# Optimization experiments

Measured on AMD Instinct MI355X. Metric: run time of the kernel, lower is better.

The kernel has to match this reference:

```python
import jax, jax.numpy as jnp
import numpy as np

N, E, IN, HID, H, G = 50000, 400000, 128, 16, 11, 64
HC = HID * H  # 176
OUT, NC = 32, 10
EPS = 1e-5


def setup_inputs() -> dict:
    key = jax.random.key(0)
    ks = jax.random.split(key, 20)
    def n(i, shape, s=0.05):
        return jax.random.normal(ks[i], shape, jnp.float32) * s
    inp = {}
    inp["x"] = jax.random.normal(ks[0], (N, IN), jnp.float32)
    inp["edge_index"] = jax.random.randint(ks[1], (2, E), 0, N, dtype=jnp.int32)
    inp["batch"] = jnp.sort(jax.random.randint(ks[2], (N,), 0, G, dtype=jnp.int32))
    inp["W_pre"] = n(3, (IN, HC)); inp["b_pre"] = jnp.zeros((HC,), jnp.float32)
    # GraphNorm params for gn_pre, gn1..gn4 stacked: [5, HC]
    inp["gn_w"] = jnp.ones((5, HC), jnp.float32)
    inp["gn_b"] = jnp.zeros((5, HC), jnp.float32)
    inp["gn_ms"] = jnp.ones((5, HC), jnp.float32)  # mean_scale
    # conv1..conv4 (concat=True) stacked params
    inp["conv_Wl"] = n(4, (4, HC, HC)); inp["conv_Wr"] = n(5, (4, HC, HC))
    inp["conv_att"] = n(6, (4, H, HID))
    inp["conv_b"] = jnp.zeros((4, HC), jnp.float32)
    inp["conv_Wres"] = n(7, (4, HC, HC))
    # conv5 (concat=False -> out dim HID)
    inp["c5_Wl"] = n(8, (HC, HC)); inp["c5_Wr"] = n(9, (HC, HC))
    inp["c5_att"] = n(10, (H, HID))
    inp["c5_b"] = jnp.zeros((HID,), jnp.float32)
    inp["c5_Wres"] = n(11, (HC, HID))
    inp["W_o1"] = n(12, (HID, HID)); inp["b_o1"] = jnp.zeros((HID,), jnp.float32)
    inp["W_o2"] = n(13, (HID, OUT)); inp["b_o2"] = jnp.zeros((OUT,), jnp.float32)
    inp["W_cls"] = n(14, (OUT, NC)); inp["b_cls"] = jnp.zeros((NC,), jnp.float32)
    return inp


def graph_norm(x, w, b, ms, batch, cnt):
    # PyG GraphNorm: out = w * (x - ms*mean) / sqrt(var + eps) + b, stats per graph
    mean = jax.ops.segment_sum(x, batch, G) / cnt  # [G, F]
    xc = x - mean[batch] * ms
    var = jax.ops.segment_sum(xc * xc, batch, G) / cnt
    std = jnp.sqrt(var + EPS)
    return w * xc / std[batch] + b


def gatv2_conv(x, Wl, Wr, att, bias, Wres, src, dst, concat):
    # src/dst already include self-loops (PyG add_self_loops=True)
    xl = (x @ Wl).reshape(N, H, -1)  # source transform [N,H,C]
    xr = (x @ Wr).reshape(N, H, -1)  # target transform [N,H,C]
    e = jax.nn.leaky_relu(xl[src] + xr[dst], 0.2)          # [E',H,C]
    alpha = jnp.einsum('ehc,hc->eh', e, att)               # [E',H]
    amax = jax.ops.segment_max(alpha, dst, N)
    amax = jnp.where(jnp.isfinite(amax), amax, 0.0)
    ex = jnp.exp(alpha - amax[dst])
    den = jax.ops.segment_sum(ex, dst, N)
    a = ex / (den[dst] + 1e-16)
    out = jax.ops.segment_sum(xl[src] * a[..., None], dst, N)  # [N,H,C]
    out = out.reshape(N, -1) if concat else out.mean(axis=1)
    return out + x @ Wres + bias


def reference(x, edge_index, batch, W_pre, b_pre, gn_w, gn_b, gn_ms,
              conv_Wl, conv_Wr, conv_att, conv_b, conv_Wres,
              c5_Wl, c5_Wr, c5_att, c5_b, c5_Wres,
              W_o1, b_o1, W_o2, b_o2, W_cls, b_cls):
    loops = jnp.arange(N, dtype=edge_index.dtype)
    src = jnp.concatenate([edge_index[0], loops])
    dst = jnp.concatenate([edge_index[1], loops])
    cnt = jax.ops.segment_sum(jnp.ones((N, 1), jnp.float32), batch, G)
    cnt = jnp.maximum(cnt, 1.0)  # guard empty graphs

    h = x @ W_pre + b_pre
    h = graph_norm(h, gn_w[0], gn_b[0], gn_ms[0], batch, cnt)
    h = jax.nn.relu(h)
    for i in range(4):
        h = gatv2_conv(h, conv_Wl[i], conv_Wr[i], conv_att[i], conv_b[i],
                       conv_Wres[i], src, dst, concat=True)
        h = graph_norm(h, gn_w[i + 1], gn_b[i + 1], gn_ms[i + 1], batch, cnt)
        h = jax.nn.relu(h)
    h = gatv2_conv(h, c5_Wl, c5_Wr, c5_att, c5_b, c5_Wres, src, dst, concat=False)
    h = jax.nn.relu(h)
    h = jax.nn.relu(h @ W_o1 + b_o1)
    h = jax.nn.relu(h @ W_o2 + b_o2)
    return h @ W_cls + b_cls
```

## Files before the change

kernel.cpp:

```cpp
#include <hip/hip_runtime.h>
#include <math.h>

#define N_NODES 50000
#define N_EDGES 400000
#define IN_F 128
#define HC 176
#define NGRAPH 64
#define NBLK_ATTN 12500
#define NCHUNK 16
#define SQOFF (NGRAPH * NCHUNK * HC)

typedef _Float16 half8 __attribute__((ext_vector_type(8)));
typedef _Float16 half4 __attribute__((ext_vector_type(4)));
typedef _Float16 half2v __attribute__((ext_vector_type(2)));
typedef float floatx4 __attribute__((ext_vector_type(4)));

__device__ inline const _Float16* urow(const _Float16* p, int c) {
  return p + (size_t)(unsigned)__builtin_amdgcn_readfirstlane(c) * HC;
}

#define PREH 45056
#define MATH 67584
#define TOT_PAIRS 495616
#define KCBYTES 22528
#define GX8 49

__global__ void prep_kernel(const float* __restrict__ Wpre,
                            const float* __restrict__ cWl, const float* __restrict__ cWr,
                            const float* __restrict__ cWres,
                            const float* __restrict__ c5Wl, const float* __restrict__ c5Wr,
                            _Float16* __restrict__ wp) {
  int gid = blockIdx.x * 256 + threadIdx.x;
  if (gid >= TOT_PAIRS) return;
  int mat, idx;
  if (gid < 22528) { mat = 0; idx = gid; }
  else { int g = gid - 22528; mat = 1 + g / 33792; idx = g % 33792; }
  int kc = idx / 5632;
  int rem = idx - kc * 5632;
  int ct = rem / 512;
  int li = rem - ct * 512;
  int lane = li >> 3, j = li & 7;
  int k = kc * 32 + ((lane >> 4) << 3) + j;
  int col = ct * 16 + (lane & 15);
  const float* src; int Ksrc; size_t base;
  if (mat == 0) { src = Wpre; Ksrc = 128; base = 0; }
  else if (mat <= 12) {
    int lm = mat - 1; int layer = lm / 3; int sub = lm - layer * 3;
    const float* s = (sub == 0) ? cWl : (sub == 1) ? cWr : cWres;
    src = s + (size_t)layer * HC * HC; Ksrc = HC;
    base = PREH + (size_t)lm * MATH;
  } else {
    src = (mat == 13) ? c5Wl : c5Wr; Ksrc = HC;
    base = PREH + (size_t)12 * MATH + (size_t)(mat - 13) * MATH;
  }
  float v = (k < Ksrc) ? src[(size_t)k * HC + col] : 0.0f;
  _Float16 h = (_Float16)v;
  _Float16 l = (_Float16)(v - (float)h);
  size_t o = base + (size_t)(kc * 11 + ct) * 1024 + li;
  wp[o] = h;
  wp[o + 512] = l;
}

template <int MINW, bool DOSTATS, bool AHALF>
__global__ __launch_bounds__(256, MINW) void gemm_mfma_t(
    const float* __restrict__ A, int M, int K, int nkc, int nmat,
    const _Float16* __restrict__ Wp, int matStride,
    const float* __restrict__ scsh, const int* __restrict__ batch,
    const float* __restrict__ bias0, const float* __restrict__ bias1,
    const float* __restrict__ bias2,
    float* __restrict__ out0, float* __restrict__ out1, float* __restrict__ out2,
    float* __restrict__ stats, int halfMask) {
  __shared__ __align__(16) char smem[2 * KCBYTES];
  const int b = blockIdx.x;
  const int grp = b >> 3, sub = b & 7;
  const int mat = grp % nmat;
  const int tile = ((grp / nmat) << 3) | sub;
  if (tile * 128 >= M) return;
  const _Float16* W = Wp + (size_t)mat * matStride;
  float* outp = (mat == 0) ? out0 : (mat == 1) ? out1 : out2;
  const float* bias = (mat == 0) ? bias0 : (mat == 1) ? bias1 : bias2;
  const bool hOut = (halfMask >> mat) & 1;
  const int tid = threadIdx.x;
  const int lane = tid & 63;
  const int wv = tid >> 6;
  const int m16 = lane & 15, quad = lane >> 4;
  const int kb = quad << 3;
  const int rowBase = tile * 128 + wv * 32;
  const int rA0 = min(rowBase + m16, M - 1);
  const int rA1 = min(rowBase + 16 + m16, M - 1);
  const float* ap0 = A + (size_t)rA0 * K + kb;
  const float* ap1 = A + (size_t)rA1 * K + kb;
  const _Float16* hp0 = (const _Float16*)A + (size_t)rA0 * K + kb;
  const _Float16* hp1 = (const _Float16*)A + (size_t)rA1 * K + kb;
  const float* sc0 = nullptr; const float* sh0 = nullptr;
  const float* sc1 = nullptr; const float* sh1 = nullptr;
  if (scsh) {
    int g0 = batch[rA0], g1 = batch[rA1];
    sc0 = scsh + (size_t)g0 * HC + kb;
    sh0 = scsh + (size_t)(NGRAPH + g0) * HC + kb;
    sc1 = scsh + (size_t)g1 * HC + kb;
    sh1 = scsh + (size_t)(NGRAPH + g1) * HC + kb;
  }

  auto stage = [&](int kc, int buf) {
    const char* src = (const char*)W + (size_t)kc * KCBYTES;
    char* dst = smem + buf * KCBYTES;
#pragma unroll
    for (int i = 0; i < 6; i++) {
      int idx = wv * 6 + i;
      if (idx < 22) {
        __builtin_amdgcn_global_load_lds(
            (const __attribute__((address_space(1))) unsigned int*)(src + idx * 1024 + lane * 16),
            (__attribute__((address_space(3))) unsigned int*)(dst + idx * 1024),
            16, 0, 0);
      }
    }
  };

  floatx4 acc0[11], acc1[11];
#pragma unroll
  for (int ct = 0; ct < 11; ct++)
#pragma unroll
    for (int r = 0; r < 4; r++) { acc0[ct][r] = 0.0f; acc1[ct][r] = 0.0f; }

  stage(0, 0);

  for (int kc = 0; kc < nkc; kc++) {
    const int buf = kc & 1;
    __syncthreads();
    if (kc + 1 < nkc) stage(kc + 1, 1 - buf);

    const int koff = kc << 5;
    float va0[8], va1[8];
    if (koff + kb + 8 <= K) {
      if (AHALF) {
        half8 u = *(const half8*)(hp0 + koff);
        half8 w = *(const half8*)(hp1 + koff);
#pragma unroll
        for (int j = 0; j < 8; j++) { va0[j] = (float)u[j]; va1[j] = (float)w[j]; }
      } else {
        float4 u0 = *(const float4*)(ap0 + koff);
        float4 u1 = *(const float4*)(ap0 + koff + 4);
        float4 w0 = *(const float4*)(ap1 + koff);
        float4 w1 = *(const float4*)(ap1 + koff + 4);
        va0[0] = u0.x; va0[1] = u0.y; va0[2] = u0.z; va0[3] = u0.w;
        va0[4] = u1.x; va0[5] = u1.y; va0[6] = u1.z; va0[7] = u1.w;
        va1[0] = w0.x; va1[1] = w0.y; va1[2] = w0.z; va1[3] = w0.w;
        va1[4] = w1.x; va1[5] = w1.y; va1[6] = w1.z; va1[7] = w1.w;
      }
      if (scsh) {
        float s0[8], h0[8], s1[8], h1[8];
        float4 t;
        t = *(const float4*)(sc0 + koff);     s0[0]=t.x; s0[1]=t.y; s0[2]=t.z; s0[3]=t.w;
        t = *(const float4*)(sc0 + koff + 4); s0[4]=t.x; s0[5]=t.y; s0[6]=t.z; s0[7]=t.w;
        t = *(const float4*)(sh0 + koff);     h0[0]=t.x; h0[1]=t.y; h0[2]=t.z; h0[3]=t.w;
        t = *(const float4*)(sh0 + koff + 4); h0[4]=t.x; h0[5]=t.y; h0[6]=t.z; h0[7]=t.w;
        t = *(const float4*)(sc1 + koff);     s1[0]=t.x; s1[1]=t.y; s1[2]=t.z; s1[3]=t.w;
        t = *(const float4*)(sc1 + koff + 4); s1[4]=t.x; s1[5]=t.y; s1[6]=t.z; s1[7]=t.w;
        t = *(const float4*)(sh1 + koff);     h1[0]=t.x; h1[1]=t.y; h1[2]=t.z; h1[3]=t.w;
        t = *(const float4*)(sh1 + koff + 4); h1[4]=t.x; h1[5]=t.y; h1[6]=t.z; h1[7]=t.w;
#pragma unroll
        for (int j = 0; j < 8; j++) {
          va0[j] = fmaxf(fmaf(va0[j], s0[j], h0[j]), 0.0f);
          va1[j] = fmaxf(fmaf(va1[j], s1[j], h1[j]), 0.0f);
        }
      }
    } else {
#pragma unroll
      for (int j = 0; j < 8; j++) { va0[j] = 0.0f; va1[j] = 0.0f; }
    }
    half8 ah0, al0, ah1, al1;
#pragma unroll
    for (int j = 0; j < 8; j++) {
      _Float16 h = (_Float16)va0[j];
      ah0[j] = h; al0[j] = (_Float16)(va0[j] - (float)h);
      _Float16 g = (_Float16)va1[j];
      ah1[j] = g; al1[j] = (_Float16)(va1[j] - (float)g);
    }
    const char* bbase = smem + buf * KCBYTES + lane * 16;
#pragma unroll
    for (int ct = 0; ct < 11; ct++) {
      half8 bh = *(const half8*)(bbase + ct * 2048);
      half8 bl = *(const half8*)(bbase + ct * 2048 + 1024);
      acc0[ct] = __builtin_amdgcn_mfma_f32_16x16x32_f16(ah0, bh, acc0[ct], 0, 0, 0);
      acc1[ct] = __builtin_amdgcn_mfma_f32_16x16x32_f16(ah1, bh, acc1[ct], 0, 0, 0);
      acc0[ct] = __builtin_amdgcn_mfma_f32_16x16x32_f16(al0, bh, acc0[ct], 0, 0, 0);
      acc1[ct] = __builtin_amdgcn_mfma_f32_16x16x32_f16(al1, bh, acc1[ct], 0, 0, 0);
      acc0[ct] = __builtin_amdgcn_mfma_f32_16x16x32_f16(ah0, bl, acc0[ct], 0, 0, 0);
      acc1[ct] = __builtin_amdgcn_mfma_f32_16x16x32_f16(ah1, bl, acc1[ct], 0, 0, 0);
    }
  }

  float bv[11];
#pragma unroll
  for (int ct = 0; ct < 11; ct++) bv[ct] = bias ? bias[ct * 16 + m16] : 0.0f;
#pragma unroll
  for (int r = 0; r < 4; r++) {
    int row0 = rowBase + (quad << 2) + r;
    if (row0 < M) {
      if (hOut) {
        _Float16* op = (_Float16*)outp + (size_t)row0 * HC + m16;
#pragma unroll
        for (int ct = 0; ct < 11; ct++) op[ct * 16] = (_Float16)(acc0[ct][r] + bv[ct]);
      } else {
        float* op = outp + (size_t)row0 * HC + m16;
#pragma unroll
        for (int ct = 0; ct < 11; ct++) op[ct * 16] = acc0[ct][r] + bv[ct];
      }
    }
    int row1 = row0 + 16;
    if (row1 < M) {
      if (hOut) {
        _Float16* op = (_Float16*)outp + (size_t)row1 * HC + m16;
#pragma unroll
        for (int ct = 0; ct < 11; ct++) op[ct * 16] = (_Float16)(acc1[ct][r] + bv[ct]);
      } else {
        float* op = outp + (size_t)row1 * HC + m16;
#pragma unroll
        for (int ct = 0; ct < 11; ct++) op[ct * 16] = acc1[ct][r] + bv[ct];
      }
    }
  }

  if (DOSTATS) {
    int gTile = batch[tile * 128];
    int lastRow = min(tile * 128 + 127, M - 1);
    bool straddle = (batch[lastRow] != gTile);
    bool validR[8]; bool otherR[8];
#pragma unroll
    for (int r = 0; r < 4; r++) {
      int row0 = rowBase + (quad << 2) + r;
      validR[r] = (row0 < M);
      otherR[r] = validR[r] && (batch[min(row0, M - 1)] != gTile);
      int row1 = row0 + 16;
      validR[4 + r] = (row1 < M);
      otherR[4 + r] = validR[4 + r] && (batch[min(row1, M - 1)] != gTile);
    }
    __syncthreads();
    float* red = (float*)smem;
#pragma unroll
    for (int ct = 0; ct < 11; ct++) {
      float sA = 0.f, qA = 0.f, sB = 0.f, qB = 0.f;
#pragma unroll
      for (int r = 0; r < 4; r++) {
        if (validR[r]) {
          float v = acc0[ct][r] + bv[ct];
          if (otherR[r]) { sB += v; qB = fmaf(v, v, qB); }
          else           { sA += v; qA = fmaf(v, v, qA); }
        }
        if (validR[4 + r]) {
          float v = acc1[ct][r] + bv[ct];
          if (otherR[4 + r]) { sB += v; qB = fmaf(v, v, qB); }
          else               { sA += v; qA = fmaf(v, v, qA); }
        }
      }
      sA += __shfl_xor(sA, 16); sA += __shfl_xor(sA, 32);
      qA += __shfl_xor(qA, 16); qA += __shfl_xor(qA, 32);
      sB += __shfl_xor(sB, 16); sB += __shfl_xor(sB, 32);
      qB += __shfl_xor(qB, 16); qB += __shfl_xor(qB, 32);
      if (quad == 0) {
        float* slot = red + (((wv * 11 + ct) * 16 + m16) << 2);
        slot[0] = sA; slot[1] = qA; slot[2] = sB; slot[3] = qB;
      }
    }
    __syncthreads();
    if (tid < HC) {
      int col = tid;
      float sA = 0.f, qA = 0.f, sB = 0.f, qB = 0.f;
#pragma unroll
      for (int w = 0; w < 4; w++) {
        float* slot = red + (((w * 11 + col / 16) * 16 + (col & 15)) << 2);
        sA += slot[0]; qA += slot[1]; sB += slot[2]; qB += slot[3];
      }
      int chunk = tile & (NCHUNK - 1);
      atomicAdd(&stats[(gTile * NCHUNK + chunk) * HC + col], sA);
      atomicAdd(&stats[SQOFF + (gTile * NCHUNK + chunk) * HC + col], qA);
      if (straddle) {
        int g2 = batch[lastRow];
        atomicAdd(&stats[(g2 * NCHUNK + chunk) * HC + col], sB);
        atomicAdd(&stats[SQOFF + (g2 * NCHUNK + chunk) * HC + col], qB);
      }
    }
  }
}

__global__ void gn_finalize_kernel(const float* __restrict__ stats, const int* __restrict__ cntInt,
                                   const float* __restrict__ gnw, const float* __restrict__ gnb,
                                   const float* __restrict__ gnms, int row,
                                   float* __restrict__ scsh) {
  int i = blockIdx.x * 256 + threadIdx.x;
  if (i >= NGRAPH * HC) return;
  int g = i / HC, f = i - g * HC;
  float sm = 0.f, sq = 0.f;
#pragma unroll
  for (int c = 0; c < NCHUNK; c++) {
    sm += stats[(g * NCHUNK + c) * HC + f];
    sq += stats[SQOFF + (g * NCHUNK + c) * HC + f];
  }
  float cnt = fmaxf((float)cntInt[g], 1.0f);
  float m = sm / cnt;
  float msq = sq / cnt;
  float ms = gnms[row * HC + f];
  float var = msq - m * m * ms * (2.0f - ms);
  float w = gnw[row * HC + f], b = gnb[row * HC + f];
  float scale = w / sqrtf(var + 1e-5f);
  float shift = b - scale * ms * m;
  scsh[i] = scale;
  scsh[NGRAPH * HC + i] = shift;
}

__global__ void cnt_bsearch_kernel(const int* __restrict__ batch, int* __restrict__ cntInt,
                                   int* __restrict__ gstart) {
  int g = threadIdx.x;
  if (g >= NGRAPH) return;
  auto lb = [&](int v) {
    int lo = 0, hi = N_NODES;
    while (lo < hi) {
      int mid = (lo + hi) >> 1;
      if (batch[mid] < v) lo = mid + 1; else hi = mid;
    }
    return lo;
  };
  int a = lb(g), b = lb(g + 1);
  cntInt[g] = b - a;
  gstart[g] = a;
  if (g == NGRAPH - 1) gstart[NGRAPH] = N_NODES;
}

__global__ void deg_hist_kernel(const int* __restrict__ dstE, int* __restrict__ deg) {
  int e = blockIdx.x * 256 + threadIdx.x;
  if (e < N_EDGES) atomicAdd(&deg[dstE[e]], 1);
}

__global__ void scan1_kernel(const int* __restrict__ deg, int* __restrict__ bsum) {
  __shared__ int sd[256];
  int i = blockIdx.x * 256 + threadIdx.x;
  sd[threadIdx.x] = (i < N_NODES) ? deg[i] : 0;
  __syncthreads();
  for (int s = 128; s > 0; s >>= 1) {
    if (threadIdx.x < s) sd[threadIdx.x] += sd[threadIdx.x + s];
    __syncthreads();
  }
  if (threadIdx.x == 0) bsum[blockIdx.x] = sd[0];
}

__global__ void scan2_kernel(int* __restrict__ bsum, int nb) {
  __shared__ int sd[256];
  int t = threadIdx.x;
  int v0 = (t < nb) ? bsum[t] : 0;
  sd[t] = v0;
  __syncthreads();
  for (int s = 1; s < 256; s <<= 1) {
    int v = (t >= s) ? sd[t - s] : 0;
    __syncthreads();
    sd[t] += v;
    __syncthreads();
  }
  if (t < nb) bsum[t] = sd[t] - v0;
}

__global__ void scan3_kernel(const int* __restrict__ deg, const int* __restrict__ bsum,
                             int* __restrict__ rowptr) {
  __shared__ int sd[256];
  int i = blockIdx.x * 256 + threadIdx.x;
  int t = threadIdx.x;
  int d = (i < N_NODES) ? deg[i] : 0;
  sd[t] = d;
  __syncthreads();
  for (int s = 1; s < 256; s <<= 1) {
    int v = (t >= s) ? sd[t - s] : 0;
    __syncthreads();
    sd[t] += v;
    __syncthreads();
  }
  if (i < N_NODES) rowptr[i] = bsum[blockIdx.x] + sd[t] - d;
  if (i == 0) rowptr[N_NODES] = N_EDGES;
}

__global__ void scatter_kernel(const int* __restrict__ srcE, const int* __restrict__ dstE,
                               const int* __restrict__ rowptr, int* __restrict__ fill,
                               int* __restrict__ colA) {
  int e = blockIdx.x * 256 + threadIdx.x;
  if (e < N_EDGES) {
    int d = dstE[e];
    int pos = rowptr[d] + atomicAdd(&fill[d], 1);
    colA[pos] = srcE[e];
  }
}

#define AEDGE(V, D, ACC)                                                      \
  do {                                                                        \
    half2v sa = (V).lo + xrl;                                                 \
    half2v sb = (V).hi + xrh;                                                 \
    sa = __builtin_elementwise_max(sa, sa * lk2);                             \
    sb = __builtin_elementwise_max(sb, sb * lk2);                             \
    float p = __builtin_amdgcn_fdot2(                                         \
        sa, ava, __builtin_amdgcn_fdot2(sb, avb, 0.0f, false), false);        \
    p += __shfl_xor(p, 1);                                                    \
    p += __shfl_xor(p, 2);                                                    \
    float pp = __expf(p);                                                     \
    (D) += pp;                                                                \
    (ACC).x = fmaf(pp, (float)(V)[0], (ACC).x);                               \
    (ACC).y = fmaf(pp, (float)(V)[1], (ACC).y);                               \
    (ACC).z = fmaf(pp, (float)(V)[2], (ACC).z);                               \
    (ACC).w = fmaf(pp, (float)(V)[3], (ACC).w);                               \
  } while (0)

#define ATTN_BODY(XLL)                                                        \
  int start = rowptr[node], end = rowptr[node + 1];                           \
  float d = 0.0f, dB = 0.0f;                                                  \
  float4 acc = make_float4(0.f, 0.f, 0.f, 0.f);                               \
  float4 accB = make_float4(0.f, 0.f, 0.f, 0.f);                              \
  half4 p1, p2;                                                               \
  if (start < end)     p1 = *(const half4*)(urow(xl, colA[start]) + (XLL));   \
  if (start + 1 < end) p2 = *(const half4*)(urow(xl, colA[start + 1]) + (XLL)); \
  {                                                                           \
    half4 svv = *(const half4*)(xl + base);                    \
    AEDGE(svv, d, acc);                                                       \
  }                                                                           \
  int j = start;                                                              \
  for (; j + 3 < end; j += 2) {                                               \
    half4 n1 = *(const half4*)(urow(xl, colA[j + 2]) + (XLL));                \
    half4 n2 = *(const half4*)(urow(xl, colA[j + 3]) + (XLL));                \
    AEDGE(p1, d, acc);                                                        \
    AEDGE(p2, dB, accB);                                                      \
    p1 = n1; p2 = n2;                                                         \
  }                                                                           \
  if (j < end)     AEDGE(p1, d, acc);                                         \
  if (j + 1 < end) AEDGE(p2, dB, accB);                                       \
  if (j + 2 < end) {                                                          \
    half4 n1 = *(const half4*)(urow(xl, colA[j + 2]) + (XLL));                \
    AEDGE(n1, d, acc);                                                        \
  }                                                                           \
  d += dB;                                                                    \
  acc.x += accB.x; acc.y += accB.y; acc.z += accB.z; acc.w += accB.w;

__global__ __launch_bounds__(256) void attn_concat_kernel(
    const _Float16* __restrict__ xl, const _Float16* __restrict__ xr,
    const float* __restrict__ att, const int* __restrict__ rowptr,
    const int* __restrict__ colA, _Float16* __restrict__ out,
    const int* __restrict__ batch, float* __restrict__ stats) {
  __shared__ float sv[4 * HC];
  int t = threadIdx.x;
  int node = blockIdx.x * 4 + (t >> 6);
  int lane = t & 63;
  if (lane < 44) {
    float4 avf = *(const float4*)(att + lane * 4);
    half2v ava, avb;
    ava[0] = (_Float16)avf.x; ava[1] = (_Float16)avf.y;
    avb[0] = (_Float16)avf.z; avb[1] = (_Float16)avf.w;
    const half2v lk2 = {(_Float16)0.2f, (_Float16)0.2f};
    size_t base = (size_t)node * HC + lane * 4;
    half4 xrv = *(const half4*)(xr + base);
    half2v xrl = xrv.lo, xrh = xrv.hi;
    half4 rv = *(const half4*)(out + base);
    ATTN_BODY(lane * 4)
    float rd = 1.0f / (d + 1e-16f);
    float4 o;
    o.x = fmaf(acc.x, rd, (float)rv[0]);
    o.y = fmaf(acc.y, rd, (float)rv[1]);
    o.z = fmaf(acc.z, rd, (float)rv[2]);
    o.w = fmaf(acc.w, rd, (float)rv[3]);
    half4 st;
    st[0] = (_Float16)o.x; st[1] = (_Float16)o.y;
    st[2] = (_Float16)o.z; st[3] = (_Float16)o.w;
    *(half4*)(out + base) = st;
    *(float4*)(&sv[(t >> 6) * HC + lane * 4]) = o;
  }
  __syncthreads();
  if (t < HC) {
    int b = blockIdx.x;
    int chunk = b & (NCHUNK - 1);
    int g0 = batch[b * 4];
    float s = 0.0f, ss = 0.0f;
    float sB = 0.0f, ssB = 0.0f;
    int gB = -1;
#pragma unroll
    for (int w = 0; w < 4; w++) {
      int g = batch[b * 4 + w];
      float v = sv[w * HC + t];
      if (g == g0) {
        s += v;
        ss = fmaf(v, v, ss);
      } else {
        gB = g; sB += v; ssB = fmaf(v, v, ssB);
      }
    }
    atomicAdd(&stats[(g0 * NCHUNK + chunk) * HC + t], s);
    atomicAdd(&stats[SQOFF + (g0 * NCHUNK + chunk) * HC + t], ss);
    if (gB >= 0) {
      atomicAdd(&stats[(gB * NCHUNK + chunk) * HC + t], sB);
      atomicAdd(&stats[SQOFF + (gB * NCHUNK + chunk) * HC + t], ssB);
    }
  }
}

__global__ __launch_bounds__(256) void attn_mean_kernel(
    const _Float16* __restrict__ xl, const _Float16* __restrict__ xr,
    const float* __restrict__ att, const int* __restrict__ rowptr,
    const int* __restrict__ colA, const float* __restrict__ res16,
    float* __restrict__ out16) {
  int t = threadIdx.x;
  int node = blockIdx.x * 4 + (t >> 6);
  int lane = t & 63;
  if (node >= N_NODES) return;
  int L = (lane < 44) ? lane : 0;
  float4 avf = *(const float4*)(att + L * 4);
  half2v ava, avb;
  ava[0] = (_Float16)avf.x; ava[1] = (_Float16)avf.y;
  avb[0] = (_Float16)avf.z; avb[1] = (_Float16)avf.w;
  const half2v lk2 = {(_Float16)0.2f, (_Float16)0.2f};
  size_t base = (size_t)node * HC + L * 4;
  half4 xrv = *(const half4*)(xr + base);
  half2v xrl = xrv.lo, xrh = xrv.hi;
  ATTN_BODY(L * 4)
  float rd = 1.0f / (d + 1e-16f);
  float4 o;
  o.x = (lane < 44) ? acc.x * rd : 0.0f;
  o.y = (lane < 44) ? acc.y * rd : 0.0f;
  o.z = (lane < 44) ? acc.z * rd : 0.0f;
  o.w = (lane < 44) ? acc.w * rd : 0.0f;
#pragma unroll
  for (int w = 4; w <= 32; w <<= 1) {
    o.x += __shfl_xor(o.x, w);
    o.y += __shfl_xor(o.y, w);
    o.z += __shfl_xor(o.z, w);
    o.w += __shfl_xor(o.w, w);
  }
  if (lane < 4) {
    const float* rp = res16 + (size_t)node * 16 + lane * 4;
    float4 r = *(const float4*)rp;
    float4 ov;
    ov.x = fmaxf(fmaf(o.x, 1.0f / 11.0f, r.x), 0.0f);
    ov.y = fmaxf(fmaf(o.y, 1.0f / 11.0f, r.y), 0.0f);
    ov.z = fmaxf(fmaf(o.z, 1.0f / 11.0f, r.z), 0.0f);
    ov.w = fmaxf(fmaf(o.w, 1.0f / 11.0f, r.w), 0.0f);
    *(float4*)(out16 + (size_t)node * 16 + lane * 4) = ov;
  }
}

__global__ __launch_bounds__(256) void res16_kernel(const _Float16* __restrict__ h,
                                                    const float* __restrict__ scsh,
                                                    const int* __restrict__ batch,
                                                    const float* __restrict__ Wres,
                                                    const float* __restrict__ b16,
                                                    float* __restrict__ res16) {
  __shared__ float Ws[176 * 16];
  __shared__ float hs[16 * 176];
  int t = threadIdx.x;
  for (int i = t; i < 176 * 16; i += 256) Ws[i] = Wres[i];
  int n0 = blockIdx.x * 16;
  for (int i = t; i < 16 * 176; i += 256) {
    int row = i / 176, k = i - row * 176;
    int g = batch[n0 + row];
    float v = (float)h[(size_t)n0 * HC + i];
    hs[i] = fmaxf(fmaf(v, scsh[g * HC + k], scsh[(NGRAPH + g) * HC + k]), 0.0f);
  }
  __syncthreads();
  int tx = t & 15, ty = t >> 4;
  float acc = b16[tx];
  for (int k = 0; k < HC; k++) acc = fmaf(hs[ty * HC + k], Ws[k * 16 + tx], acc);
  res16[(size_t)(n0 + ty) * 16 + tx] = acc;
}

__global__ __launch_bounds__(256) void head_kernel(
    const float* __restrict__ in16, const float* __restrict__ Wo1,
    const float* __restrict__ bo1, const float* __restrict__ Wo2,
    const float* __restrict__ bo2, const float* __restrict__ Wc,
    const float* __restrict__ bc, float* __restrict__ outp) {
  __shared__ float w1[256], w2[512], wcS[320], b1[16], b2[32], bcS[10];
  int t = threadIdx.x;
  for (int i = t; i < 256; i += 256) w1[i] = Wo1[i];
  for (int i = t; i < 512; i += 256) w2[i] = Wo2[i];
  for (int i = t; i < 320; i += 256) wcS[i] = Wc[i];
  if (t < 16) b1[t] = bo1[t];
  if (t < 32) b2[t] = bo2[t];
  if (t < 10) bcS[t] = bc[t];
  __syncthreads();
  int n = blockIdx.x * 256 + t;
  if (n >= N_NODES) return;
  float x[16];
#pragma unroll
  for (int i = 0; i < 16; i++) x[i] = in16[(size_t)n * 16 + i];
  float o1[16];
#pragma unroll
  for (int j = 0; j < 16; j++) {
    float a = b1[j];
#pragma unroll
    for (int k = 0; k < 16; k++) a = fmaf(x[k], w1[k * 16 + j], a);
    o1[j] = fmaxf(a, 0.0f);
  }
  float o2[32];
#pragma unroll
  for (int j = 0; j < 32; j++) {
    float a = b2[j];
#pragma unroll
    for (int k = 0; k < 16; k++) a = fmaf(o1[k], w2[k * 32 + j], a);
    o2[j] = fmaxf(a, 0.0f);
  }
#pragma unroll
  for (int j = 0; j < 10; j++) {
    float a = bcS[j];
#pragma unroll
    for (int k = 0; k < 32; k++) a = fmaf(o2[k], wcS[k * 10 + j], a);
    outp[(size_t)n * 10 + j] = a;
  }
}

extern "C" void kernel_launch(void* const* d_in, const int* in_sizes, int n_in,
                              void* d_out, int out_size, void* d_ws, size_t ws_size,
                              hipStream_t stream) {
  (void)in_sizes; (void)n_in; (void)out_size; (void)ws_size;
  const float* x     = (const float*)d_in[0];
  const int*   ei    = (const int*)d_in[1];
  const int*   srcE  = ei;
  const int*   dstE  = ei + N_EDGES;
  const int*   batch = (const int*)d_in[2];
  const float* W_pre = (const float*)d_in[3];
  const float* b_pre = (const float*)d_in[4];
  const float* gn_w  = (const float*)d_in[5];
  const float* gn_b  = (const float*)d_in[6];
  const float* gn_ms = (const float*)d_in[7];
  const float* cWl   = (const float*)d_in[8];
  const float* cWr   = (const float*)d_in[9];
  const float* cAtt  = (const float*)d_in[10];
  const float* cB    = (const float*)d_in[11];
  const float* cWres = (const float*)d_in[12];
  const float* c5Wl  = (const float*)d_in[13];
  const float* c5Wr  = (const float*)d_in[14];
  const float* c5Att = (const float*)d_in[15];
  const float* c5b   = (const float*)d_in[16];
  const float* c5Wres= (const float*)d_in[17];
  const float* Wo1   = (const float*)d_in[18];
  const float* bo1   = (const float*)d_in[19];
  const float* Wo2   = (const float*)d_in[20];
  const float* bo2   = (const float*)d_in[21];
  const float* Wc    = (const float*)d_in[22];
  const float* bc    = (const float*)d_in[23];

  const size_t FB = (size_t)N_NODES * HC;
  const size_t STB2 = (size_t)2 * NGRAPH * NCHUNK * HC;
  float* ws    = (float*)d_ws;
  float* buf0  = ws;
  float* buf1  = ws + FB;
  float* buf2  = ws + 2 * FB;
  float* buf3  = ws + 3 * FB;
  float* res16 = ws + 4 * FB;
  float* out16 = res16 + (size_t)N_NODES * 16;
  float* stats2 = out16 + (size_t)N_NODES * 16;
  int* deg     = (int*)(stats2 + 5 * STB2);
  int* fill    = deg + N_NODES;
  float* scsh  = (float*)(fill + N_NODES);
  _Float16* wph = (_Float16*)(scsh + (size_t)2 * NGRAPH * HC);
  int* ibase   = (int*)((char*)wph + (size_t)991232 * 2);
  int* cntInt  = ibase;
  int* gstart  = ibase + 64;
  int* rowptr  = gstart + 65;
  int* colA    = rowptr + N_NODES + 1;
  int* bsum    = colA + N_EDGES;

  const int NB = (N_NODES + 255) / 256;

  hipMemsetAsync(stats2, 0, sizeof(float) * 5 * STB2 + sizeof(int) * 2 * N_NODES, stream);

  prep_kernel<<<(TOT_PAIRS + 255) / 256, 256, 0, stream>>>(W_pre, cWl, cWr, cWres, c5Wl, c5Wr, wph);
  cnt_bsearch_kernel<<<1, 64, 0, stream>>>(batch, cntInt, gstart);
  deg_hist_kernel<<<(N_EDGES + 255) / 256, 256, 0, stream>>>(dstE, deg);
  scan1_kernel<<<NB, 256, 0, stream>>>(deg, bsum);
  scan2_kernel<<<1, 256, 0, stream>>>(bsum, NB);
  scan3_kernel<<<NB, 256, 0, stream>>>(deg, bsum, rowptr);
  scatter_kernel<<<(N_EDGES + 255) / 256, 256, 0, stream>>>(srcE, dstE, rowptr, fill, colA);

  gemm_mfma_t<2, true, false><<<GX8 * 1 * 8, 256, 0, stream>>>(
      x, N_NODES, IN_F, 4, 1, wph, 0, nullptr, batch,
      b_pre, nullptr, nullptr, buf0, nullptr, nullptr,
      stats2, 1);
  gn_finalize_kernel<<<(NGRAPH * HC + 255) / 256, 256, 0, stream>>>(stats2, cntInt, gn_w, gn_b, gn_ms, 0, scsh);

  float* h = buf0;
  float* o = buf3;
  for (int i = 0; i < 4; i++) {
    const _Float16* Wcat_i = wph + PREH + (size_t)(3 * i) * MATH;
    gemm_mfma_t<3, false, true><<<GX8 * 3 * 8, 256, 0, stream>>>(
        h, N_NODES, HC, 6, 3, Wcat_i, MATH, scsh, batch,
        nullptr, nullptr, cB + i * HC, buf1, buf2, o,
        nullptr, 7);
    float* st = stats2 + (size_t)(i + 1) * STB2;
    attn_concat_kernel<<<NBLK_ATTN, 256, 0, stream>>>((const _Float16*)buf1, (const _Float16*)buf2,
                                                      cAtt + i * HC,
                                                      rowptr, colA, (_Float16*)o, batch, st);
    gn_finalize_kernel<<<(NGRAPH * HC + 255) / 256, 256, 0, stream>>>(st, cntInt, gn_w, gn_b, gn_ms, i + 1, scsh);
    float* tmp = h; h = o; o = tmp;
  }

  const _Float16* Wc5 = wph + PREH + (size_t)12 * MATH;
  gemm_mfma_t<3, false, true><<<GX8 * 2 * 8, 256, 0, stream>>>(
      h, N_NODES, HC, 6, 2, Wc5, MATH, scsh, batch,
      nullptr, nullptr, nullptr, buf1, buf2, nullptr,
      nullptr, 3);
  res16_kernel<<<N_NODES / 16, 256, 0, stream>>>((const _Float16*)h, scsh, batch, c5Wres, c5b, res16);
  attn_mean_kernel<<<(N_NODES + 3) / 4, 256, 0, stream>>>((const _Float16*)buf1, (const _Float16*)buf2,
                                                          c5Att, rowptr, colA, res16, out16);

  head_kernel<<<NB, 256, 0, stream>>>(out16, Wo1, bo1, Wo2, bo2, Wc, bc, (float*)d_out);
}
```

Before: 645.9 us.

## Single-buffer weight LDS, prefetch A registers, raise GEMM occupancy bound

The GEMM drops from double-buffered to single-buffered LDS for weight chunks, halving shared memory. The next chunk is staged only after the MFMA loop finishes, behind an extra barrier. To hide global latency, the A-row loads for the next k-chunk are prefetched into registers one iteration ahead. The launch bound's minimum waves for the conv GEMMs rises from 3 to 4, aiming for more resident blocks. The trade-off is that weight staging no longer overlaps compute within a block and there is an extra sync per chunk, while register pressure grows under a tighter occupancy bound.

```diff
diff --git a/kernel.cpp b/kernel.cpp
--- a/kernel.cpp
+++ b/kernel.cpp
@@ -70,7 +70,7 @@
     const float* __restrict__ bias2,
     float* __restrict__ out0, float* __restrict__ out1, float* __restrict__ out2,
     float* __restrict__ stats, int halfMask) {
-  __shared__ __align__(16) char smem[2 * KCBYTES];
+  __shared__ __align__(16) char smem[KCBYTES];
   const int b = blockIdx.x;
   const int grp = b >> 3, sub = b & 7;
   const int mat = grp % nmat;
@@ -102,16 +102,15 @@
     sh1 = scsh + (size_t)(NGRAPH + g1) * HC + kb;
   }
 
-  auto stage = [&](int kc, int buf) {
+  auto stage = [&](int kc) {
     const char* src = (const char*)W + (size_t)kc * KCBYTES;
-    char* dst = smem + buf * KCBYTES;
 #pragma unroll
     for (int i = 0; i < 6; i++) {
       int idx = wv * 6 + i;
       if (idx < 22) {
         __builtin_amdgcn_global_load_lds(
             (const __attribute__((address_space(1))) unsigned int*)(src + idx * 1024 + lane * 16),
-            (__attribute__((address_space(3))) unsigned int*)(dst + idx * 1024),
+            (__attribute__((address_space(3))) unsigned int*)(smem + idx * 1024),
             16, 0, 0);
       }
     }
@@ -123,30 +122,50 @@
 #pragma unroll
     for (int r = 0; r < 4; r++) { acc0[ct][r] = 0.0f; acc1[ct][r] = 0.0f; }
 
-  stage(0, 0);
+  stage(0);
+
+  half8 pU = {}, pW = {};
+  float4 pu0 = {0,0,0,0}, pu1 = {0,0,0,0}, pw0 = {0,0,0,0}, pw1 = {0,0,0,0};
+  if (AHALF) {
+    pU = *(const half8*)(hp0);
+    pW = *(const half8*)(hp1);
+  } else {
+    pu0 = *(const float4*)(ap0);
+    pu1 = *(const float4*)(ap0 + 4);
+    pw0 = *(const float4*)(ap1);
+    pw1 = *(const float4*)(ap1 + 4);
+  }
 
   for (int kc = 0; kc < nkc; kc++) {
-    const int buf = kc & 1;
-    __syncthreads();
-    if (kc + 1 < nkc) stage(kc + 1, 1 - buf);
-
     const int koff = kc << 5;
+    const bool valid = (koff + kb + 8 <= K);
+    half8 cU = pU, cW = pW;
+    float4 cu0 = pu0, cu1 = pu1, cw0 = pw0, cw1 = pw1;
+    if (kc + 1 < nkc) {
+      const int koff2 = (kc + 1) << 5;
+      if (koff2 + kb + 8 <= K) {
+        if (AHALF) {
+          pU = *(const half8*)(hp0 + koff2);
+          pW = *(const half8*)(hp1 + koff2);
+        } else {
+          pu0 = *(const float4*)(ap0 + koff2);
+          pu1 = *(const float4*)(ap0 + koff2 + 4);
+          pw0 = *(const float4*)(ap1 + koff2);
+          pw1 = *(const float4*)(ap1 + koff2 + 4);
+        }
+      }
+    }
+
     float va0[8], va1[8];
-    if (koff + kb + 8 <= K) {
+    if (valid) {
       if (AHALF) {
-        half8 u = *(const half8*)(hp0 + koff);
-        half8 w = *(const half8*)(hp1 + koff);
-#pragma unroll
-        for (int j = 0; j < 8; j++) { va0[j] = (float)u[j]; va1[j] = (float)w[j]; }
+#pragma unroll
+        for (int j = 0; j < 8; j++) { va0[j] = (float)cU[j]; va1[j] = (float)cW[j]; }
       } else {
-        float4 u0 = *(const float4*)(ap0 + koff);
-        float4 u1 = *(const float4*)(ap0 + koff + 4);
-        float4 w0 = *(const float4*)(ap1 + koff);
-        float4 w1 = *(const float4*)(ap1 + koff + 4);
-        va0[0] = u0.x; va0[1] = u0.y; va0[2] = u0.z; va0[3] = u0.w;
-        va0[4] = u1.x; va0[5] = u1.y; va0[6] = u1.z; va0[7] = u1.w;
-        va1[0] = w0.x; va1[1] = w0.y; va1[2] = w0.z; va1[3] = w0.w;
-        va1[4] = w1.x; va1[5] = w1.y; va1[6] = w1.z; va1[7] = w1.w;
+        va0[0] = cu0.x; va0[1] = cu0.y; va0[2] = cu0.z; va0[3] = cu0.w;
+        va0[4] = cu1.x; va0[5] = cu1.y; va0[6] = cu1.z; va0[7] = cu1.w;
+        va1[0] = cw0.x; va1[1] = cw0.y; va1[2] = cw0.z; va1[3] = cw0.w;
+        va1[4] = cw1.x; va1[5] = cw1.y; va1[6] = cw1.z; va1[7] = cw1.w;
       }
       if (scsh) {
         float s0[8], h0[8], s1[8], h1[8];
@@ -177,7 +196,9 @@
       _Float16 g = (_Float16)va1[j];
       ah1[j] = g; al1[j] = (_Float16)(va1[j] - (float)g);
     }
-    const char* bbase = smem + buf * KCBYTES + lane * 16;
+
+    __syncthreads();
+    const char* bbase = smem + lane * 16;
 #pragma unroll
     for (int ct = 0; ct < 11; ct++) {
       half8 bh = *(const half8*)(bbase + ct * 2048);
@@ -189,6 +210,8 @@
       acc0[ct] = __builtin_amdgcn_mfma_f32_16x16x32_f16(ah0, bl, acc0[ct], 0, 0, 0);
       acc1[ct] = __builtin_amdgcn_mfma_f32_16x16x32_f16(ah1, bl, acc1[ct], 0, 0, 0);
     }
+    __syncthreads();
+    if (kc + 1 < nkc) stage(kc + 1);
   }
 
   float bv[11];
@@ -681,7 +704,7 @@
   float* o = buf3;
   for (int i = 0; i < 4; i++) {
     const _Float16* Wcat_i = wph + PREH + (size_t)(3 * i) * MATH;
-    gemm_mfma_t<3, false, true><<<GX8 * 3 * 8, 256, 0, stream>>>(
+    gemm_mfma_t<4, false, true><<<GX8 * 3 * 8, 256, 0, stream>>>(
         h, N_NODES, HC, 6, 3, Wcat_i, MATH, scsh, batch,
         nullptr, nullptr, cB + i * HC, buf1, buf2, o,
         nullptr, 7);
@@ -694,7 +717,7 @@
   }
 
   const _Float16* Wc5 = wph + PREH + (size_t)12 * MATH;
-  gemm_mfma_t<3, false, true><<<GX8 * 2 * 8, 256, 0, stream>>>(
+  gemm_mfma_t<4, false, true><<<GX8 * 2 * 8, 256, 0, stream>>>(
       h, N_NODES, HC, 6, 2, Wc5, MATH, scsh, batch,
       nullptr, nullptr, nullptr, buf1, buf2, nullptr,
       nullptr, 3);
```

New measurement: 978.6 us. +51.5%, slower.
